# Kernel tuning notes

Hardware: AMD Instinct MI355X
Metric: run time of the kernel (lower is better)

Reference implementation:

```python
import jax, jax.numpy as jnp
import numpy as np

N_NODES = 100000
N_EDGES = 1600000
IN_F, HID, OUT = 256, 32, 16


def setup_inputs() -> dict:
    key = jax.random.key(0)
    ks = jax.random.split(key, 10)
    x = jax.random.normal(ks[0], (N_NODES, IN_F), dtype=jnp.float32)
    edge_index = jax.random.randint(ks[1], (2, N_EDGES), 0, N_NODES, dtype=jnp.int32)
    s = lambda fan_in: 1.0 / np.sqrt(fan_in)
    # Linear params stored torch-style: weight [out, in], bias [out]
    w1a_w = jax.random.uniform(ks[2], (HID, IN_F), jnp.float32, -s(IN_F), s(IN_F))
    w1a_b = jax.random.uniform(ks[3], (HID,), jnp.float32, -s(IN_F), s(IN_F))
    w1b_w = jax.random.uniform(ks[4], (HID, HID), jnp.float32, -s(HID), s(HID))
    w1b_b = jax.random.uniform(ks[5], (HID,), jnp.float32, -s(HID), s(HID))
    w2a_w = jax.random.uniform(ks[6], (OUT, HID), jnp.float32, -s(HID), s(HID))
    w2a_b = jax.random.uniform(ks[7], (OUT,), jnp.float32, -s(HID), s(HID))
    w2b_w = jax.random.uniform(ks[8], (OUT, OUT), jnp.float32, -s(OUT), s(OUT))
    w2b_b = jax.random.uniform(ks[9], (OUT,), jnp.float32, -s(OUT), s(OUT))
    return {"x": x, "w1a_w": w1a_w, "w1a_b": w1a_b, "w1b_w": w1b_w, "w1b_b": w1b_b,
            "w2a_w": w2a_w, "w2a_b": w2a_b, "w2b_w": w2b_w, "w2b_b": w2b_b,
            "edge_index": edge_index}


def _simple_layer(x, wa_w, wa_b, wb_w, wb_b, src, dst):
    h = x @ wa_w.T + wa_b                         # [N, out_ch]
    f_new = h @ wb_w.T + wb_b                     # [N, out_ch]
    agg = jax.ops.segment_sum(h[src], dst, num_segments=x.shape[0])
    return f_new + agg


def reference(x, w1a_w, w1a_b, w1b_w, w1b_b, w2a_w, w2a_b, w2b_w, w2b_b, edge_index):
    src, dst = edge_index[0], edge_index[1]
    h = _simple_layer(x, w1a_w, w1a_b, w1b_w, w1b_b, src, dst)
    h = jax.nn.relu(h)
    # dropout is identity in eval mode (training=False)
    h = _simple_layer(h, w2a_w, w2a_b, w2b_w, w2b_b, src, dst)
    return jax.nn.log_softmax(h, axis=1)
```

## Files before the change

### kernel.cpp

```cpp
#include <hip/hip_runtime.h>
#include <hip/hip_bf16.h>
#include <math.h>

#define N_NODES 100000
#define N_EDGES 1600000
#define IN_F 256
#define HID 32
#define OUTC 16
#define NBUCK 1000
#define BUCK_W 100
#define NBB 256
#define CHUNK 6250
#define MAXE 4096
#define K1_BLOCKS ((N_NODES + 63) / 64)

typedef unsigned short ushort_t;
typedef unsigned int uint_t;
typedef __attribute__((ext_vector_type(8))) short bf16x8;
typedef __attribute__((ext_vector_type(4))) float f32x4;

__device__ inline ushort_t f2bf(float f) {
    union { float f; uint_t u; } v; v.f = f;
    uint_t r = v.u + 0x7fff + ((v.u >> 16) & 1);
    return (ushort_t)(r >> 16);
}
__device__ inline float bf2f(ushort_t h) {
    union { uint_t u; float f; } v; v.u = (uint_t)h << 16;
    return v.f;
}
__device__ inline float bf_lo(uint_t d) {
    union { uint_t u; float f; } v; v.u = d << 16;
    return v.f;
}
__device__ inline float bf_hi(uint_t d) {
    union { uint_t u; float f; } v; v.u = d & 0xFFFF0000u;
    return v.f;
}
__device__ inline bf16x8 packA(const float4& lo, const float4& hi) {
    bf16x8 a;
    a[0] = (short)f2bf(lo.x); a[1] = (short)f2bf(lo.y);
    a[2] = (short)f2bf(lo.z); a[3] = (short)f2bf(lo.w);
    a[4] = (short)f2bf(hi.x); a[5] = (short)f2bf(hi.y);
    a[6] = (short)f2bf(hi.z); a[7] = (short)f2bf(hi.w);
    return a;
}
__device__ inline void gload_lds16(const void* g, void* l) {
    __builtin_amdgcn_global_load_lds((const __attribute__((address_space(1))) void*)g,
                                     (__attribute__((address_space(3))) void*)l, 16, 0, 0);
}

__global__ __launch_bounds__(256) void k_cnt_wfuse(
    const int* __restrict__ ei, int* __restrict__ bhist,
    const float* __restrict__ w1a_w, const float* __restrict__ w1a_b,
    const float* __restrict__ w1b_w, const float* __restrict__ w1b_b,
    ushort_t* __restrict__ wpack, float* __restrict__ bp)
{
    __shared__ char smem[32 * 1024 + 4 * 1024 + 256];
    const int t = threadIdx.x;

    if (blockIdx.x < NBB) {
        int* lh = (int*)smem;
        const int blk = blockIdx.x;
        for (int b = t; b < NBUCK; b += 256) lh[b] = 0;
        __syncthreads();
        const int base = blk * CHUNK;
        for (int i = t; i < CHUNK; i += 256) {
            const int dst = ei[N_EDGES + base + i];
            atomicAdd(&lh[dst / BUCK_W], 1);
        }
        __syncthreads();
        for (int b = t; b < NBUCK; b += 256) bhist[b * NBB + blk] = lh[b];
        return;
    }

    float (*wps)[256] = (float (*)[256])smem;
    float (*wb_s)[32] = (float (*)[32])(smem + 32 * 1024);
    float* ba_s       = (float*)(smem + 36 * 1024);
    for (int i = t; i < 1024; i += 256) wb_s[i >> 5][i & 31] = w1b_w[i];
    if (t < 32) ba_s[t] = w1a_b[t];
    __syncthreads();
    const int k = t;
    for (int o = 0; o < 32; ++o) {
        float s = 0.f;
        #pragma unroll 8
        for (int c = 0; c < 32; ++c) s += wb_s[o][c] * w1a_w[c * 256 + k];
        wps[o][k] = s;
    }
    if (t < 32) {
        float s = 0.f;
        for (int c = 0; c < 32; ++c) s += wb_s[t][c] * ba_s[c];
        bp[t] = s + w1b_b[t];
    }
    __syncthreads();
    for (int idx = t; idx < 4 * 8 * 64 * 8; idx += 256) {
        const int j  = idx & 7;
        const int l  = (idx >> 3) & 63;
        const int ks = (idx >> 9) & 7;
        const int q  = idx >> 12;
        const int ncol = ((q & 1) << 4) + (l & 15);
        const int krow = ks * 32 + ((l >> 4) << 3) + j;
        const float v = (q < 2) ? w1a_w[ncol * 256 + krow] : wps[ncol][krow];
        wpack[idx] = f2bf(v);
    }
}

__global__ __launch_bounds__(256) void k_scanH(const int* __restrict__ bhist,
                                               int* __restrict__ boffB, int* __restrict__ btot)
{
    __shared__ int sh[256];
    const int t = threadIdx.x;
    const int b = blockIdx.x;
    const int v = bhist[b * NBB + t];
    sh[t] = v;
    __syncthreads();
    #pragma unroll
    for (int off = 1; off < 256; off <<= 1) {
        const int u = (t >= off) ? sh[t - off] : 0;
        __syncthreads();
        sh[t] += u;
        __syncthreads();
    }
    boffB[b * NBB + t] = sh[t] - v;
    if (t == 255) btot[b] = sh[255];
}

__global__ __launch_bounds__(1024) void k_scanH2(const int* __restrict__ btot,
                                                 int* __restrict__ bstart)
{
    __shared__ int sh[1024];
    const int t = threadIdx.x;
    const int v = (t < NBUCK) ? btot[t] : 0;
    sh[t] = v;
    __syncthreads();
    #pragma unroll
    for (int off = 1; off < 1024; off <<= 1) {
        const int u = (t >= off) ? sh[t - off] : 0;
        __syncthreads();
        sh[t] += u;
        __syncthreads();
    }
    if (t < NBUCK) bstart[t] = sh[t] - v;
    if (t == NBUCK - 1) bstart[NBUCK] = sh[t];
}

__global__ __launch_bounds__(256) void k_scat_k1(
    const int* __restrict__ ei,
    const int* __restrict__ boffB, const int* __restrict__ bstart,
    int* __restrict__ pairsP,
    const float* __restrict__ x,
    const float* __restrict__ w1a_b, const float* __restrict__ bp,
    const ushort_t* __restrict__ wpack,
    ushort_t* __restrict__ h1b, float* __restrict__ out1)
{
    __shared__ uint4 arena4[4096];
    const int t = threadIdx.x;

    if (blockIdx.x < NBB) {
        int* lcur = (int*)arena4;
        const int blk = blockIdx.x;
        for (int b = t; b < NBUCK; b += 256) lcur[b] = bstart[b] + boffB[b * NBB + blk];
        __syncthreads();
        const int base = blk * CHUNK;
        for (int i = t; i < CHUNK; i += 256) {
            const int src = ei[base + i];
            const int dst = ei[N_EDGES + base + i];
            const int b = dst / BUCK_W;
            const int pos = atomicAdd(&lcur[b], 1);
            pairsP[pos] = ((dst - b * BUCK_W) << 17) | src;
        }
        return;
    }

    char* arena = (char*)arena4;
    const int l64 = t & 63;
    const int wv  = t >> 6;
    const int node0 = (int)(blockIdx.x - NBB) * 64;

    #pragma unroll
    for (int i = 0; i < 16; ++i) {
        const int n = i * 4 + wv;
        int gn = node0 + n;
        if (gn >= N_NODES) gn = N_NODES - 1;
        const char* gsrc = (const char*)x + (size_t)gn * 1024
                         + (size_t)((l64 ^ (n & 7)) * 16);
        char* ldst = arena + (size_t)n * 1024;
        gload_lds16(gsrc, ldst);
    }
    __syncthreads();

    const int arow = l64 & 15;
    const int kq   = l64 >> 4;
    const int nn   = wv * 16 + arow;
    const bf16x8* wf = (const bf16x8*)wpack;

    f32x4 accA0 = {0.f, 0.f, 0.f, 0.f};
    f32x4 accA1 = {0.f, 0.f, 0.f, 0.f};
    f32x4 accB0 = {0.f, 0.f, 0.f, 0.f};
    f32x4 accB1 = {0.f, 0.f, 0.f, 0.f};

    const char* xrow = arena + (size_t)nn * 1024;
    const int sw = nn & 7;

    #pragma unroll
    for (int ks = 0; ks < 8; ++ks) {
        const int u0 = ks * 8 + kq * 2;
        const float4 xlo = *(const float4*)(xrow + ((u0 ^ sw) * 16));
        const float4 xhi = *(const float4*)(xrow + (((u0 + 1) ^ sw) * 16));
        const bf16x8 a = packA(xlo, xhi);
        const bf16x8 bA0 = wf[(0 * 8 + ks) * 64 + l64];
        const bf16x8 bA1 = wf[(1 * 8 + ks) * 64 + l64];
        const bf16x8 bB0 = wf[(2 * 8 + ks) * 64 + l64];
        const bf16x8 bB1 = wf[(3 * 8 + ks) * 64 + l64];
        accA0 = __builtin_amdgcn_mfma_f32_16x16x32_bf16(a, bA0, accA0, 0, 0, 0);
        accA1 = __builtin_amdgcn_mfma_f32_16x16x32_bf16(a, bA1, accA1, 0, 0, 0);
        accB0 = __builtin_amdgcn_mfma_f32_16x16x32_bf16(a, bB0, accB0, 0, 0, 0);
        accB1 = __builtin_amdgcn_mfma_f32_16x16x32_bf16(a, bB1, accB1, 0, 0, 0);
    }

    const int ch = l64 & 15;
    const int rbase = (l64 >> 4) * 4;
    const float ba0 = w1a_b[ch];
    const float ba1 = w1a_b[ch + 16];
    const float bb0 = bp[ch];
    const float bb1 = bp[ch + 16];

    #pragma unroll
    for (int r = 0; r < 4; ++r) {
        const int node = node0 + wv * 16 + rbase + r;
        if (node < N_NODES) {
            h1b[(size_t)node * HID + ch]       = f2bf(accA0[r] + ba0);
            h1b[(size_t)node * HID + ch + 16]  = f2bf(accA1[r] + ba1);
            out1[(size_t)node * HID + ch]      = accB0[r] + bb0;
            out1[(size_t)node * HID + ch + 16] = accB1[r] + bb1;
        }
    }
}

__global__ __launch_bounds__(512) void k_agg32(const int* __restrict__ bstart,
                                               const int* __restrict__ pairsP,
                                               const ushort_t* __restrict__ h1b,
                                               float* __restrict__ out1,
                                               int* __restrict__ colg,
                                               int* __restrict__ offg)
{
    __shared__ int cnt[128];
    __shared__ int off[129];
    __shared__ int srt[MAXE];
    const int t = threadIdx.x;
    const int b = blockIdx.x;
    const int c2 = t & 15;
    const int grp = t >> 4;
    const uint_t* h1u = (const uint_t*)h1b;

    const int e0g = bstart[b];
    const int e1g = bstart[b + 1];
    const bool single = (e1g - e0g) <= MAXE;

    for (int ch0 = e0g; ch0 < e1g; ch0 += MAXE) {
        const int ce = (ch0 + MAXE < e1g) ? (ch0 + MAXE) : e1g;
        const int cn = ce - ch0;

        if (t < 128) cnt[t] = 0;
        __syncthreads();
        for (int i = t; i < cn; i += 512)
            atomicAdd(&cnt[pairsP[ch0 + i] >> 17], 1);
        __syncthreads();
        {
            int v = (t < 128) ? cnt[t] : 0;
            if (t < 128) off[t] = v;
            __syncthreads();
            #pragma unroll
            for (int o = 1; o < 128; o <<= 1) {
                int u = 0;
                if (t < 128 && t >= o) u = off[t - o];
                __syncthreads();
                if (t < 128) off[t] += u;
                __syncthreads();
            }
            if (t < 128) {
                const int inc = off[t];
                off[t] = inc - v;
                cnt[t] = inc - v;
                if (t == 127) off[128] = inc;
            }
        }
        __syncthreads();
        for (int i = t; i < cn; i += 512) {
            const int p = pairsP[ch0 + i];
            const int pos = atomicAdd(&cnt[p >> 17], 1);
            srt[pos] = p & 0x1FFFF;
        }
        __syncthreads();
        if (single) {
            for (int i = t; i < cn; i += 512) colg[ch0 + i] = srt[i];
            if (t <= BUCK_W) offg[b * (BUCK_W + 1) + t] = e0g + off[t];
        }
        for (int n = grp; n < BUCK_W; n += 32) {
            const int e0 = off[n];
            const int e1 = off[n + 1];
            float l0 = 0.f, h0 = 0.f, l1 = 0.f, h1 = 0.f;
            int e = e0;
            for (; e + 4 <= e1; e += 4) {
                const uint_t u0 = h1u[(size_t)srt[e]     * 16 + c2];
                const uint_t u1 = h1u[(size_t)srt[e + 1] * 16 + c2];
                const uint_t u2 = h1u[(size_t)srt[e + 2] * 16 + c2];
                const uint_t u3 = h1u[(size_t)srt[e + 3] * 16 + c2];
                l0 += bf_lo(u0); h0 += bf_hi(u0);
                l1 += bf_lo(u1); h1 += bf_hi(u1);
                l0 += bf_lo(u2); h0 += bf_hi(u2);
                l1 += bf_lo(u3); h1 += bf_hi(u3);
            }
            for (; e < e1; ++e) {
                const uint_t u = h1u[(size_t)srt[e] * 16 + c2];
                l0 += bf_lo(u); h0 += bf_hi(u);
            }
            float2* o = (float2*)&out1[((size_t)b * BUCK_W + n) * HID + 2 * c2];
            const float2 cur = *o;
            float2 nv;
            nv.x = fmaxf(cur.x + l0 + l1, 0.f);
            nv.y = fmaxf(cur.y + h0 + h1, 0.f);
            *o = nv;
        }
        __syncthreads();
    }
}

__global__ __launch_bounds__(256) void k3_layer2_dense(
    const float* __restrict__ out1,
    const float* __restrict__ w2a_w, const float* __restrict__ w2a_b,
    const float* __restrict__ w2b_w, const float* __restrict__ w2b_b,
    ushort_t* __restrict__ h2b, float* __restrict__ out2)
{
    __shared__ float rs[64][33];
    __shared__ float h2s[64][17];
    __shared__ float wa[16][33];
    __shared__ float wb[16][17];

    const int t = threadIdx.x;
    const int node0 = blockIdx.x * 64;
    const int nrem = N_NODES - node0;

    for (int i = t; i < 16 * 32; i += 256)
        wa[i >> 5][i & 31] = w2a_w[i];
    if (t < 16 * 16) wb[t >> 4][t & 15] = w2b_w[t];
    for (int i = t; i < 64 * 32; i += 256) {
        int r = i >> 5, c = i & 31;
        float v = 0.f;
        if (r < nrem) v = out1[(size_t)(node0 + r) * HID + c];
        rs[r][c] = fmaxf(v, 0.f);
    }
    __syncthreads();

    const int o = t & 15;
    const int g = t >> 4;

    const float ba = w2a_b[o];
    float acc[4] = {};
    for (int c = 0; c < 32; ++c) {
        const float w = wa[o][c];
        #pragma unroll
        for (int j = 0; j < 4; ++j) acc[j] += rs[g * 4 + j][c] * w;
    }
    #pragma unroll
    for (int j = 0; j < 4; ++j) {
        const int ln = g * 4 + j;
        const float v = acc[j] + ba;
        h2s[ln][o] = v;
        if (ln < nrem) h2b[(size_t)(node0 + ln) * OUTC + o] = f2bf(v);
    }
    __syncthreads();

    const float bbv = w2b_b[o];
    float f[4] = {};
    for (int c = 0; c < 16; ++c) {
        const float w = wb[o][c];
        #pragma unroll
        for (int j = 0; j < 4; ++j) f[j] += h2s[g * 4 + j][c] * w;
    }
    #pragma unroll
    for (int j = 0; j < 4; ++j) {
        const int ln = g * 4 + j;
        if (ln < nrem) out2[(size_t)(node0 + ln) * OUTC + o] = f[j] + bbv;
    }
}

__global__ __launch_bounds__(512) void k_agg16_sm(const int* __restrict__ bstart,
                                                  const int* __restrict__ pairsP,
                                                  const int* __restrict__ colg,
                                                  const int* __restrict__ offg,
                                                  const ushort_t* __restrict__ h2b,
                                                  float* __restrict__ out2)
{
    const int t = threadIdx.x;
    const int b = blockIdx.x;
    const int e0g = bstart[b];
    const int e1g = bstart[b + 1];
    const uint_t* h2u = (const uint_t*)h2b;

    if (e1g - e0g <= MAXE) {
        const int c2 = t & 7;
        const int grp = t >> 3;
        const int ob = b * (BUCK_W + 1);
        for (int n = grp; n < BUCK_W; n += 64) {
            const int e0 = offg[ob + n];
            const int e1 = offg[ob + n + 1];
            float l0 = 0.f, h0 = 0.f, l1 = 0.f, h1v = 0.f;
            int e = e0;
            for (; e + 4 <= e1; e += 4) {
                const uint_t u0 = h2u[(size_t)colg[e]     * 8 + c2];
                const uint_t u1 = h2u[(size_t)colg[e + 1] * 8 + c2];
                const uint_t u2 = h2u[(size_t)colg[e + 2] * 8 + c2];
                const uint_t u3 = h2u[(size_t)colg[e + 3] * 8 + c2];
                l0 += bf_lo(u0); h0 += bf_hi(u0);
                l1 += bf_lo(u1); h1v += bf_hi(u1);
                l0 += bf_lo(u2); h0 += bf_hi(u2);
                l1 += bf_lo(u3); h1v += bf_hi(u3);
            }
            for (; e < e1; ++e) {
                const uint_t u = h2u[(size_t)colg[e] * 8 + c2];
                l0 += bf_lo(u); h0 += bf_hi(u);
            }

            float2* op = (float2*)&out2[((size_t)b * BUCK_W + n) * OUTC + 2 * c2];
            const float2 cur = *op;
            const float v0 = cur.x + l0 + l1;
            const float v1 = cur.y + h0 + h1v;

            float m = fmaxf(v0, v1);
            #pragma unroll
            for (int o = 4; o > 0; o >>= 1)
                m = fmaxf(m, __shfl_xor(m, o, 8));
            float s = expf(v0 - m) + expf(v1 - m);
            #pragma unroll
            for (int o = 4; o > 0; o >>= 1)
                s += __shfl_xor(s, o, 8);
            const float lse = m + logf(s);
            float2 nv; nv.x = v0 - lse; nv.y = v1 - lse;
            *op = nv;
        }
        return;
    }

    __shared__ int cnt[128];
    __shared__ int off[129];
    __shared__ int srt[MAXE];
    const int c = t & 15;
    const int grp = t >> 4;

    for (int ch0 = e0g; ch0 < e1g; ch0 += MAXE) {
        const int ce = (ch0 + MAXE < e1g) ? (ch0 + MAXE) : e1g;
        const int cn = ce - ch0;
        const bool last = (ce == e1g);

        if (t < 128) cnt[t] = 0;
        __syncthreads();
        for (int i = t; i < cn; i += 512)
            atomicAdd(&cnt[pairsP[ch0 + i] >> 17], 1);
        __syncthreads();
        {
            int v = (t < 128) ? cnt[t] : 0;
            if (t < 128) off[t] = v;
            __syncthreads();
            #pragma unroll
            for (int o = 1; o < 128; o <<= 1) {
                int u = 0;
                if (t < 128 && t >= o) u = off[t - o];
                __syncthreads();
                if (t < 128) off[t] += u;
                __syncthreads();
            }
            if (t < 128) {
                const int inc = off[t];
                off[t] = inc - v;
                cnt[t] = inc - v;
                if (t == 127) off[128] = inc;
            }
        }
        __syncthreads();
        for (int i = t; i < cn; i += 512) {
            const int p = pairsP[ch0 + i];
            const int pos = atomicAdd(&cnt[p >> 17], 1);
            srt[pos] = p & 0x1FFFF;
        }
        __syncthreads();

        for (int n = grp; n < BUCK_W; n += 32) {
            const int e0 = off[n];
            const int e1 = off[n + 1];
            float acc = 0.f, acc2 = 0.f;
            int e = e0;
            for (; e + 1 < e1; e += 2) {
                acc += bf2f(h2b[(size_t)srt[e] * OUTC + c]);
                acc2 += bf2f(h2b[(size_t)srt[e + 1] * OUTC + c]);
            }
            if (e < e1) acc += bf2f(h2b[(size_t)srt[e] * OUTC + c]);
            acc += acc2;

            const size_t oidx = ((size_t)b * BUCK_W + n) * OUTC + c;
            if (!last) {
                out2[oidx] += acc;
            } else {
                const float val = out2[oidx] + acc;
                float m = val;
                #pragma unroll
                for (int o = 8; o > 0; o >>= 1)
                    m = fmaxf(m, __shfl_xor(m, o, 16));
                float s = expf(val - m);
                #pragma unroll
                for (int o = 8; o > 0; o >>= 1)
                    s += __shfl_xor(s, o, 16);
                const float lse = m + logf(s);
                out2[oidx] = val - lse;
            }
        }
        __syncthreads();
    }
}

extern "C" void kernel_launch(void* const* d_in, const int* in_sizes, int n_in,
                              void* d_out, int out_size, void* d_ws, size_t ws_size,
                              hipStream_t stream)
{
    const float* x      = (const float*)d_in[0];
    const float* w1a_w  = (const float*)d_in[1];
    const float* w1a_b  = (const float*)d_in[2];
    const float* w1b_w  = (const float*)d_in[3];
    const float* w1b_b  = (const float*)d_in[4];
    const float* w2a_w  = (const float*)d_in[5];
    const float* w2a_b  = (const float*)d_in[6];
    const float* w2b_w  = (const float*)d_in[7];
    const float* w2b_b  = (const float*)d_in[8];
    const int*   ei     = (const int*)d_in[9];
    float* out = (float*)d_out;

    float*    out1   = (float*)d_ws;
    ushort_t* h1b    = (ushort_t*)(out1 + (size_t)N_NODES * HID);
    ushort_t* h2b    = h1b + (size_t)N_NODES * HID;
    int*      pairsP = (int*)(h2b + (size_t)N_NODES * OUTC);
    ushort_t* wpack  = (ushort_t*)(pairsP + N_EDGES);
    float*    bp     = (float*)(wpack + 4 * 8 * 64 * 8);
    int*      bhist  = (int*)(bp + 32);
    int*      boffB  = bhist + NBUCK * NBB;
    int*      btot   = boffB + NBUCK * NBB;
    int*      bstart = btot + NBUCK;
    int*      colg   = bstart + NBUCK + 1;
    int*      offg   = colg + N_EDGES;

    k_cnt_wfuse<<<NBB + 1, 256, 0, stream>>>(ei, bhist,
                                             w1a_w, w1a_b, w1b_w, w1b_b, wpack, bp);
    k_scanH <<<NBUCK, 256, 0, stream>>>(bhist, boffB, btot);
    k_scanH2<<<1, 1024, 0, stream>>>(btot, bstart);
    k_scat_k1<<<NBB + K1_BLOCKS, 256, 0, stream>>>(ei, boffB, bstart, pairsP,
                                                   x, w1a_b, bp, wpack, h1b, out1);
    k_agg32<<<NBUCK, 512, 0, stream>>>(bstart, pairsP, h1b, out1, colg, offg);
    k3_layer2_dense<<<(N_NODES + 63) / 64, 256, 0, stream>>>(out1, w2a_w, w2a_b, w2b_w, w2b_b, h2b, out);
    k_agg16_sm<<<NBUCK, 512, 0, stream>>>(bstart, pairsP, colg, offg, h2b, out);
}
```

Before: 141.0 us.

## Make layer-1 GEMM blocks persistent with double-buffered x staging and LDS weights

The dense layer-1 part of k_scat_k1 now runs as 256 persistent blocks instead of one block per 64 nodes. Each block copies the packed bf16 weights into LDS once, then walks 32-node tiles while prefetching the next tile of x into a second LDS buffer. The four waves split the work by weight half (h1 vs out1) and by 16-row half, so each wave issues two MFMAs per k-step instead of four. The goal is to overlap the x stream with compute and avoid reloading weights from global memory per block. The cost is 96KB of LDS per block, which limits occupancy to very few waves per CU, and the overlap only holds if the async-load waits do not serialize the prefetch.

```diff
diff --git a/kernel.cpp b/kernel.cpp
--- a/kernel.cpp
+++ b/kernel.cpp
@@ -12,7 +12,8 @@
 #define NBB 256
 #define CHUNK 6250
 #define MAXE 4096
-#define K1_BLOCKS ((N_NODES + 63) / 64)
+#define NTILES 3125
+#define K1P 256
 
 typedef unsigned short ushort_t;
 typedef unsigned int uint_t;
@@ -152,7 +153,7 @@
     const ushort_t* __restrict__ wpack,
     ushort_t* __restrict__ h1b, float* __restrict__ out1)
 {
-    __shared__ uint4 arena4[4096];
+    __shared__ uint4 arena4[6144];
     const int t = threadIdx.x;
 
     if (blockIdx.x < NBB) {
@@ -171,69 +172,85 @@
         return;
     }
 
-    char* arena = (char*)arena4;
+    bf16x8* wl = (bf16x8*)arena4;
+
+    {
+        const uint4* src = (const uint4*)wpack;
+        #pragma unroll
+        for (int i = 0; i < 8; ++i) arena4[t + i * 256] = src[t + i * 256];
+    }
+
     const int l64 = t & 63;
     const int wv  = t >> 6;
-    const int node0 = (int)(blockIdx.x - NBB) * 64;
-
-    #pragma unroll
-    for (int i = 0; i < 16; ++i) {
-        const int n = i * 4 + wv;
-        int gn = node0 + n;
-        if (gn >= N_NODES) gn = N_NODES - 1;
-        const char* gsrc = (const char*)x + (size_t)gn * 1024
-                         + (size_t)((l64 ^ (n & 7)) * 16);
-        char* ldst = arena + (size_t)n * 1024;
-        gload_lds16(gsrc, ldst);
-    }
-    __syncthreads();
-
+    const int pb  = (int)blockIdx.x - NBB;
+
+    #define STAGE_X(bufc, tt)                                                     \
+    {                                                                             \
+        const int node0_ = (tt) * 32;                                             \
+        char* xbase_ = (char*)arena4 + 32768 + (bufc) * 32768;                    \
+        _Pragma("unroll")                                                         \
+        for (int i_ = 0; i_ < 8; ++i_) {                                          \
+            const int n_ = i_ * 4 + wv;                                           \
+            int gn_ = node0_ + n_;                                                \
+            if (gn_ >= N_NODES) gn_ = N_NODES - 1;                                \
+            const char* gsrc_ = (const char*)x + (size_t)gn_ * 1024               \
+                              + (size_t)((l64 ^ (n_ & 7)) * 16);                  \
+            gload_lds16(gsrc_, xbase_ + (size_t)n_ * 1024);                       \
+        }                                                                         \
+    }
+
+    const int q = wv >> 1;
+    const int s = wv & 1;
     const int arow = l64 & 15;
-    const int kq   = l64 >> 4;
-    const int nn   = wv * 16 + arow;
-    const bf16x8* wf = (const bf16x8*)wpack;
-
-    f32x4 accA0 = {0.f, 0.f, 0.f, 0.f};
-    f32x4 accA1 = {0.f, 0.f, 0.f, 0.f};
-    f32x4 accB0 = {0.f, 0.f, 0.f, 0.f};
-    f32x4 accB1 = {0.f, 0.f, 0.f, 0.f};
-
-    const char* xrow = arena + (size_t)nn * 1024;
+    const int kq = l64 >> 4;
+    const int nn = s * 16 + arow;
     const int sw = nn & 7;
-
-    #pragma unroll
-    for (int ks = 0; ks < 8; ++ks) {
-        const int u0 = ks * 8 + kq * 2;
-        const float4 xlo = *(const float4*)(xrow + ((u0 ^ sw) * 16));
-        const float4 xhi = *(const float4*)(xrow + (((u0 + 1) ^ sw) * 16));
-        const bf16x8 a = packA(xlo, xhi);
-        const bf16x8 bA0 = wf[(0 * 8 + ks) * 64 + l64];
-        const bf16x8 bA1 = wf[(1 * 8 + ks) * 64 + l64];
-        const bf16x8 bB0 = wf[(2 * 8 + ks) * 64 + l64];
-        const bf16x8 bB1 = wf[(3 * 8 + ks) * 64 + l64];
-        accA0 = __builtin_amdgcn_mfma_f32_16x16x32_bf16(a, bA0, accA0, 0, 0, 0);
-        accA1 = __builtin_amdgcn_mfma_f32_16x16x32_bf16(a, bA1, accA1, 0, 0, 0);
-        accB0 = __builtin_amdgcn_mfma_f32_16x16x32_bf16(a, bB0, accB0, 0, 0, 0);
-        accB1 = __builtin_amdgcn_mfma_f32_16x16x32_bf16(a, bB1, accB1, 0, 0, 0);
-    }
-
     const int ch = l64 & 15;
     const int rbase = (l64 >> 4) * 4;
-    const float ba0 = w1a_b[ch];
-    const float ba1 = w1a_b[ch + 16];
-    const float bb0 = bp[ch];
-    const float bb1 = bp[ch + 16];
-
-    #pragma unroll
-    for (int r = 0; r < 4; ++r) {
-        const int node = node0 + wv * 16 + rbase + r;
-        if (node < N_NODES) {
-            h1b[(size_t)node * HID + ch]       = f2bf(accA0[r] + ba0);
-            h1b[(size_t)node * HID + ch + 16]  = f2bf(accA1[r] + ba1);
-            out1[(size_t)node * HID + ch]      = accB0[r] + bb0;
-            out1[(size_t)node * HID + ch + 16] = accB1[r] + bb1;
-        }
-    }
+    const float b0 = q ? bp[ch]      : w1a_b[ch];
+    const float b1 = q ? bp[ch + 16] : w1a_b[ch + 16];
+
+    int ti = pb;
+    int cur = 0;
+    if (ti < NTILES) STAGE_X(0, ti)
+
+    for (; ti < NTILES; ti += K1P) {
+        __syncthreads();
+        const int tn = ti + K1P;
+        if (tn < NTILES) STAGE_X(cur ^ 1, tn)
+
+        const char* xrow = (const char*)arena4 + 32768 + cur * 32768 + (size_t)nn * 1024;
+        f32x4 acc0 = {0.f, 0.f, 0.f, 0.f};
+        f32x4 acc1 = {0.f, 0.f, 0.f, 0.f};
+        #pragma unroll
+        for (int ks = 0; ks < 8; ++ks) {
+            const int u0 = ks * 8 + kq * 2;
+            const float4 xlo = *(const float4*)(xrow + ((u0 ^ sw) * 16));
+            const float4 xhi = *(const float4*)(xrow + (((u0 + 1) ^ sw) * 16));
+            const bf16x8 a = packA(xlo, xhi);
+            const bf16x8 bf0 = wl[((q * 2) * 8 + ks) * 64 + l64];
+            const bf16x8 bf1 = wl[((q * 2 + 1) * 8 + ks) * 64 + l64];
+            acc0 = __builtin_amdgcn_mfma_f32_16x16x32_bf16(a, bf0, acc0, 0, 0, 0);
+            acc1 = __builtin_amdgcn_mfma_f32_16x16x32_bf16(a, bf1, acc1, 0, 0, 0);
+        }
+
+        const int nodeb = ti * 32 + s * 16 + rbase;
+        #pragma unroll
+        for (int r = 0; r < 4; ++r) {
+            const int node = nodeb + r;
+            if (node < N_NODES) {
+                if (q == 0) {
+                    h1b[(size_t)node * HID + ch]      = f2bf(acc0[r] + b0);
+                    h1b[(size_t)node * HID + ch + 16] = f2bf(acc1[r] + b1);
+                } else {
+                    out1[(size_t)node * HID + ch]      = acc0[r] + b0;
+                    out1[(size_t)node * HID + ch + 16] = acc1[r] + b1;
+                }
+            }
+        }
+        cur ^= 1;
+    }
+    #undef STAGE_X
 }
 
 __global__ __launch_bounds__(512) void k_agg32(const int* __restrict__ bstart,
@@ -550,8 +567,8 @@
                                              w1a_w, w1a_b, w1b_w, w1b_b, wpack, bp);
     k_scanH <<<NBUCK, 256, 0, stream>>>(bhist, boffB, btot);
     k_scanH2<<<1, 1024, 0, stream>>>(btot, bstart);
-    k_scat_k1<<<NBB + K1_BLOCKS, 256, 0, stream>>>(ei, boffB, bstart, pairsP,
-                                                   x, w1a_b, bp, wpack, h1b, out1);
+    k_scat_k1<<<NBB + K1P, 256, 0, stream>>>(ei, boffB, bstart, pairsP,
+                                             x, w1a_b, bp, wpack, h1b, out1);
     k_agg32<<<NBUCK, 512, 0, stream>>>(bstart, pairsP, h1b, out1, colg, offg);
     k3_layer2_dense<<<(N_NODES + 63) / 64, 256, 0, stream>>>(out1, w2a_w, w2a_b, w2b_w, w2b_b, h2b, out);
     k_agg16_sm<<<NBUCK, 512, 0, stream>>>(bstart, pairsP, colg, offg, h2b, out);
```

Result: no change. 140.8 us (-0.1%).
